# Kernel optimization log

Hardware: AMD Instinct MI355X
Metric: run time of the kernel (lower is better)

## Reference

```python
import jax, jax.numpy as jnp
import numpy as np

N, NFEAT, NHID, NHEADS = 4096, 512, 64, 8
P = 65536
ALPHA = 0.2  # LeakyReLU negative slope
NEG = -9e15  # mask value used by standard dense GAT


def setup_inputs() -> dict:
    key = jax.random.key(0)
    ks = jax.random.split(key, 9)
    x = jax.random.normal(ks[0], (N, NFEAT), dtype=jnp.float32)
    adj = (jax.random.uniform(ks[1], (N, N)) < 0.01).astype(jnp.float32)  # sparse-ish binary graph
    s = 0.05
    W_heads = jax.random.normal(ks[2], (NHEADS, NFEAT, NHID), dtype=jnp.float32) * s
    a_heads = jax.random.normal(ks[3], (NHEADS, 2 * NHID), dtype=jnp.float32) * s
    W_out = jax.random.normal(ks[4], (NHID * NHEADS, NHID), dtype=jnp.float32) * s
    a_out = jax.random.normal(ks[5], (2 * NHID,), dtype=jnp.float32) * s
    W_score = jax.random.normal(ks[6], (NHID, NHID), dtype=jnp.float32) * s
    pair1_idx = jax.random.randint(ks[7], (P,), 0, N, dtype=jnp.int32)
    pair2_idx = jax.random.randint(ks[8], (P,), 0, N, dtype=jnp.int32)
    return dict(x=x, adj=adj, W_heads=W_heads, a_heads=a_heads,
                W_out=W_out, a_out=a_out, W_score=W_score,
                pair1_idx=pair1_idx, pair2_idx=pair2_idx)


def _gat_layer(h, adj, W, a, concat):
    # Standard dense GraphAttentionLayer (no dropout: eval mode)
    Wh = h @ W                       # [N, out]
    out = W.shape[1]
    e_src = Wh @ a[:out]             # [N]
    e_dst = Wh @ a[out:]             # [N]
    e = jax.nn.leaky_relu(e_src[:, None] + e_dst[None, :], ALPHA)  # [N, N]
    logits = jnp.where(adj > 0, e, NEG)
    attn = jax.nn.softmax(logits, axis=1)
    hp = attn @ Wh                   # [N, out]
    return jax.nn.elu(hp) if concat else hp


def reference(x, adj, W_heads, a_heads, W_out, a_out, W_score, pair1_idx, pair2_idx):
    # multi-head layer, vmapped over heads; each head: [N, NHID]
    heads = jax.vmap(lambda W, a: _gat_layer(x, adj, W, a, True))(W_heads, a_heads)
    h = jnp.transpose(heads, (1, 0, 2)).reshape(N, NHEADS * NHID)  # concat dim=1
    h = jax.nn.elu(_gat_layer(h, adj, W_out, a_out, False))        # [N, NHID]
    embed1 = h[pair1_idx]            # sparse.mm(pair1_map, h) == row gather
    embed2 = h[pair2_idx]
    # diag(embed1 @ W_score @ embed2.T) == rowwise dot
    scores = jnp.sum((embed1 @ W_score) * embed2, axis=1)  # [P]
    return scores
```

## Files before the change

kernel.cpp:

```cpp
#include <hip/hip_runtime.h>
#include <math.h>

#define N 4096
#define NFEAT 512
#define NHID 64
#define NHEADS 8
#define P_PAIRS 65536
#define CAP 128
#define LRELU_ALPHA 0.2f
#define GEMM_BLOCKS 256
#define CSR_BLOCKS 512

typedef short bf16x8 __attribute__((ext_vector_type(8)));
typedef float f32x4 __attribute__((ext_vector_type(4)));

__device__ __forceinline__ unsigned short f2bf(float f) {
  unsigned u = __float_as_uint(f);
  u = u + 0x7FFFu + ((u >> 16) & 1u);
  return (unsigned short)(u >> 16);
}
__device__ __forceinline__ float bf2f(unsigned short h) {
  return __uint_as_float(((unsigned)h) << 16);
}

__device__ __forceinline__ int swz(int row, int s) {
  int sl = ((row & 7) * 32 + s) ^ ((row & 7) << 3);
  return (row >> 3) * 256 + sl;
}

__global__ __launch_bounds__(256) void prep_wt(const float* __restrict__ W1,
                                               const float* __restrict__ W2,
                                               unsigned short* __restrict__ w1hi,
                                               unsigned short* __restrict__ w1lo,
                                               unsigned short* __restrict__ w2hi,
                                               unsigned short* __restrict__ w2lo) {
  int c = blockIdx.x;
  const float* W;
  unsigned short *hiP, *loP;
  if (c < 512) { W = W1; hiP = w1hi; loP = w1lo; }
  else         { W = W2; hiP = w2hi; loP = w2lo; c -= 512; }
  const float* Wp = W + (size_t)(c >> 6) * 512 * 64 + (c & 63);
  for (int k = threadIdx.x; k < 512; k += 256) {
    float v = Wp[(size_t)k * 64];
    unsigned short hb = f2bf(v);
    hiP[(size_t)c * 512 + k] = hb;
    loP[(size_t)c * 512 + k] = f2bf(v - bf2f(hb));
  }
}

template <bool F32A>
__device__ __forceinline__ void gemm_body(unsigned short* As, unsigned short* Bs,
                                          int mIdx, int head,
                                          const float* __restrict__ Af,
                                          const unsigned short* __restrict__ Ahi,
                                          const unsigned short* __restrict__ Alo,
                                          const unsigned short* __restrict__ Bhi,
                                          const unsigned short* __restrict__ Blo,
                                          const float* __restrict__ aVec,
                                          float* __restrict__ C,
                                          float* __restrict__ esrc,
                                          float* __restrict__ edst,
                                          float* __restrict__ cpart) {
  const int t = threadIdx.x;
  const int m0 = mIdx * 128;
  const int c0 = head * 64;
  const int lane = t & 63, wave = t >> 6;
  const int g = lane >> 4, r = lane & 15;
  const int wm = (wave >> 1) * 32;
  const int wn = (wave & 1) * 32;
  const int sar = t >> 2, sak = (t & 3) * 8;
  const int tb = t & 255;
  const int sbr = tb >> 2, sbk = (tb & 3) * 8;
  const unsigned short* Bsel = (t < 256) ? Bhi : Blo;
  const int bhalf = (t < 256) ? 0 : 1;
  const int idxA = swz(sar, sak);
  const int idxB = swz(sbr, sbk);
  const size_t aOff = (size_t)(m0 + sar) * 512 + sak;
  const size_t bOff = (size_t)(c0 + sbr) * 512 + sbk;
  const f32x4 z = {0.f, 0.f, 0.f, 0.f};
  f32x4 acc[2][2];
  acc[0][0] = z; acc[0][1] = z; acc[1][0] = z; acc[1][1] = z;

  int4 a0, a1, b0;
  auto loadRegs = [&](int kb) {
    if constexpr (F32A) {
      float4 v0 = *(const float4*)(Af + aOff + kb);
      float4 v1 = *(const float4*)(Af + aOff + kb + 4);
      unsigned h0 = f2bf(v0.x), h1 = f2bf(v0.y), h2 = f2bf(v0.z), h3 = f2bf(v0.w);
      unsigned h4 = f2bf(v1.x), h5 = f2bf(v1.y), h6 = f2bf(v1.z), h7 = f2bf(v1.w);
      unsigned l0 = f2bf(v0.x - bf2f(h0)), l1 = f2bf(v0.y - bf2f(h1));
      unsigned l2 = f2bf(v0.z - bf2f(h2)), l3 = f2bf(v0.w - bf2f(h3));
      unsigned l4 = f2bf(v1.x - bf2f(h4)), l5 = f2bf(v1.y - bf2f(h5));
      unsigned l6 = f2bf(v1.z - bf2f(h6)), l7 = f2bf(v1.w - bf2f(h7));
      a0.x = h0 | (h1 << 16); a0.y = h2 | (h3 << 16);
      a0.z = h4 | (h5 << 16); a0.w = h6 | (h7 << 16);
      a1.x = l0 | (l1 << 16); a1.y = l2 | (l3 << 16);
      a1.z = l4 | (l5 << 16); a1.w = l6 | (l7 << 16);
    } else {
      a0 = *(const int4*)(Ahi + aOff + kb);
      a1 = *(const int4*)(Alo + aOff + kb);
    }
    b0 = *(const int4*)(Bsel + bOff + kb);
  };
  auto storeLds = [&](int buf) {
    *(int4*)(&As[(buf * 2 + 0) * 4096 + idxA]) = a0;
    *(int4*)(&As[(buf * 2 + 1) * 4096 + idxA]) = a1;
    *(int4*)(&Bs[(buf * 2 + bhalf) * 2048 + idxB]) = b0;
  };

  loadRegs(0);
  storeLds(0);
  __syncthreads();

  for (int ch = 0; ch < 16; ++ch) {
    const int cur = ch & 1;
    if (ch < 15) loadRegs((ch + 1) * 32);
    bf16x8 ah[2], al[2], bh[2], bl[2];
#pragma unroll
    for (int f = 0; f < 2; ++f) {
      int ia = swz(wm + f * 16 + r, 8 * g);
      int ib = swz(wn + f * 16 + r, 8 * g);
      ah[f] = *(const bf16x8*)(&As[(cur * 2 + 0) * 4096 + ia]);
      al[f] = *(const bf16x8*)(&As[(cur * 2 + 1) * 4096 + ia]);
      bh[f] = *(const bf16x8*)(&Bs[(cur * 2 + 0) * 2048 + ib]);
      bl[f] = *(const bf16x8*)(&Bs[(cur * 2 + 1) * 2048 + ib]);
    }
#pragma unroll
    for (int i = 0; i < 2; ++i)
#pragma unroll
      for (int j = 0; j < 2; ++j) {
        acc[i][j] = __builtin_amdgcn_mfma_f32_16x16x32_bf16(ah[i], bh[j], acc[i][j], 0, 0, 0);
        acc[i][j] = __builtin_amdgcn_mfma_f32_16x16x32_bf16(al[i], bh[j], acc[i][j], 0, 0, 0);
        acc[i][j] = __builtin_amdgcn_mfma_f32_16x16x32_bf16(ah[i], bl[j], acc[i][j], 0, 0, 0);
      }
    if (ch < 15) {
      storeLds(cur ^ 1);
      __syncthreads();
    }
  }

  __syncthreads();
  float* Cs = (float*)As;
#pragma unroll
  for (int i = 0; i < 2; ++i)
#pragma unroll
    for (int j = 0; j < 2; ++j)
#pragma unroll
      for (int q = 0; q < 4; ++q)
        Cs[(wm + i * 16 + 4 * g + q) * 64 + wn + j * 16 + r] = acc[i][j][q];
  __syncthreads();
  float* Cp = C + ((size_t)head * N + m0) * 64;
  const float* aV = aVec + (size_t)head * 128;
  float as_ = aV[lane], ad_ = aV[64 + lane];
  float cs = 0.f;
#pragma unroll
  for (int rr = 0; rr < 16; ++rr) {
    int row = wave * 16 + rr;
    float v = Cs[row * 64 + lane];
    Cp[(size_t)row * 64 + lane] = v;
    cs += v;
    float s = v * as_, d = v * ad_;
#pragma unroll
    for (int off = 32; off; off >>= 1) {
      s += __shfl_xor(s, off);
      d += __shfl_xor(d, off);
    }
    if (lane == 0) {
      esrc[(size_t)head * N + m0 + row] = s;
      edst[(size_t)head * N + m0 + row] = d;
    }
  }
  float* red = (float*)Bs;
  red[wave * 64 + lane] = cs;
  __syncthreads();
  if (wave == 0) {
    float s = 0.f;
#pragma unroll
    for (int j = 0; j < 8; ++j) s += red[j * 64 + lane];
    cpart[((size_t)head * 32 + mIdx) * 64 + lane] = s;
  }
}

__global__ __launch_bounds__(512) void front(const float* __restrict__ x,
                                             const float* __restrict__ adj,
                                             const unsigned short* __restrict__ w1hi,
                                             const unsigned short* __restrict__ w1lo,
                                             const float* __restrict__ aVec,
                                             float* __restrict__ Wh1,
                                             float* __restrict__ es1,
                                             float* __restrict__ ed1,
                                             float* __restrict__ cpart1,
                                             int* __restrict__ counts,
                                             int* __restrict__ cols) {
  __shared__ unsigned short As[2 * 2 * 4096];
  __shared__ unsigned short Bs[2 * 2 * 2048];
  int b = blockIdx.x;
  if (b >= GEMM_BLOCKS) {
    int lane = threadIdx.x & 63;
    int row = (b - GEMM_BLOCKS) * 8 + (threadIdx.x >> 6);
    const float4* arow = (const float4*)(adj + (size_t)row * N);
    int* crow = cols + (size_t)row * CAP;
    unsigned long long below = (1ULL << lane) - 1;
    int cnt = 0;
#pragma unroll 4
    for (int it = 0; it < 16; ++it) {
      float4 v = arow[it * 64 + lane];
      int base = (it * 64 + lane) * 4;
#pragma unroll
      for (int j = 0; j < 4; ++j) {
        float f = (j == 0) ? v.x : (j == 1) ? v.y : (j == 2) ? v.z : v.w;
        unsigned long long mask = __ballot(f > 0.f);
        if (f > 0.f) {
          int pos = cnt + __popcll(mask & below);
          if (pos < CAP) crow[pos] = base + j;
        }
        cnt += __popcll(mask);
      }
    }
    if (lane == 0) counts[row] = cnt < CAP ? cnt : CAP;
    return;
  }
  gemm_body<true>(As, Bs, b & 31, b >> 5, x, nullptr, nullptr, w1hi, w1lo,
                  aVec, Wh1, es1, ed1, cpart1);
}

__global__ __launch_bounds__(256) void gat_attn_l1(const float* __restrict__ Wh,
                                                   const float* __restrict__ esrc,
                                                   const float* __restrict__ edst,
                                                   const int* __restrict__ counts,
                                                   const int* __restrict__ cols,
                                                   const float* __restrict__ cpart1,
                                                   unsigned short* __restrict__ hhi,
                                                   unsigned short* __restrict__ hlo) {
  int h = blockIdx.x & 7;
  int wv = threadIdx.x >> 6;
  int lane = threadIdx.x & 63;
  int sg = lane >> 4, sl = lane & 15;
  int i = (blockIdx.x >> 3) * 4 + wv;
  int cnt = counts[i];
  __shared__ int jls[4][CAP];
  __shared__ float pls[4][CAP];
  const float* WhH = Wh + (size_t)h * N * 64;
  float4 acc = {0.f, 0.f, 0.f, 0.f};
  if (cnt == 0) {
    float4 sv = {0.f, 0.f, 0.f, 0.f};
    for (int j = 0; j < 32; ++j) {
      float4 p = *(const float4*)(cpart1 + ((size_t)h * 32 + j) * 64 + 4 * sl);
      sv.x += p.x; sv.y += p.y; sv.z += p.z; sv.w += p.w;
    }
    acc.x = sv.x * (1.0f / N); acc.y = sv.y * (1.0f / N);
    acc.z = sv.z * (1.0f / N); acc.w = sv.w * (1.0f / N);
  } else {
    const int* cl = cols + (size_t)i * CAP;
    jls[wv][lane] = (lane < cnt) ? cl[lane] : 0;
    jls[wv][lane + 64] = (lane + 64 < cnt) ? cl[lane + 64] : 0;
    float ei = esrc[h * N + i];
    const float* ed = edst + (size_t)h * N;
    float e0 = -1e30f, e1 = -1e30f;
    if (lane < cnt) {
      float e = ei + ed[jls[wv][lane]];
      e0 = (e > 0.f) ? e : LRELU_ALPHA * e;
    }
    if (lane + 64 < cnt) {
      float e = ei + ed[jls[wv][lane + 64]];
      e1 = (e > 0.f) ? e : LRELU_ALPHA * e;
    }
    float m = fmaxf(e0, e1);
#pragma unroll
    for (int off = 32; off; off >>= 1) m = fmaxf(m, __shfl_xor(m, off));
    float p0 = (lane < cnt) ? __expf(e0 - m) : 0.f;
    float p1 = (lane + 64 < cnt) ? __expf(e1 - m) : 0.f;
    float ssum = p0 + p1;
#pragma unroll
    for (int off = 32; off; off >>= 1) ssum += __shfl_xor(ssum, off);
    pls[wv][lane] = p0;
    pls[wv][lane + 64] = p1;
    int L = (cnt + 15) & ~15;
    for (int k = 0; k < L; k += 16) {
      int j0 = jls[wv][k + sg];
      int j1 = jls[wv][k + 4 + sg];
      int j2 = jls[wv][k + 8 + sg];
      int j3 = jls[wv][k + 12 + sg];
      float4 v0 = *(const float4*)(WhH + ((size_t)j0 << 6) + 4 * sl);
      float4 v1 = *(const float4*)(WhH + ((size_t)j1 << 6) + 4 * sl);
      float4 v2 = *(const float4*)(WhH + ((size_t)j2 << 6) + 4 * sl);
      float4 v3 = *(const float4*)(WhH + ((size_t)j3 << 6) + 4 * sl);
      float q0 = pls[wv][k + sg];
      float q1 = pls[wv][k + 4 + sg];
      float q2 = pls[wv][k + 8 + sg];
      float q3 = pls[wv][k + 12 + sg];
      acc.x = fmaf(q0, v0.x, acc.x); acc.y = fmaf(q0, v0.y, acc.y);
      acc.z = fmaf(q0, v0.z, acc.z); acc.w = fmaf(q0, v0.w, acc.w);
      acc.x = fmaf(q1, v1.x, acc.x); acc.y = fmaf(q1, v1.y, acc.y);
      acc.z = fmaf(q1, v1.z, acc.z); acc.w = fmaf(q1, v1.w, acc.w);
      acc.x = fmaf(q2, v2.x, acc.x); acc.y = fmaf(q2, v2.y, acc.y);
      acc.z = fmaf(q2, v2.z, acc.z); acc.w = fmaf(q2, v2.w, acc.w);
      acc.x = fmaf(q3, v3.x, acc.x); acc.y = fmaf(q3, v3.y, acc.y);
      acc.z = fmaf(q3, v3.z, acc.z); acc.w = fmaf(q3, v3.w, acc.w);
    }
    acc.x += __shfl_xor(acc.x, 16); acc.y += __shfl_xor(acc.y, 16);
    acc.z += __shfl_xor(acc.z, 16); acc.w += __shfl_xor(acc.w, 16);
    acc.x += __shfl_xor(acc.x, 32); acc.y += __shfl_xor(acc.y, 32);
    acc.z += __shfl_xor(acc.z, 32); acc.w += __shfl_xor(acc.w, 32);
    float inv = 1.0f / ssum;
    acc.x *= inv; acc.y *= inv; acc.z *= inv; acc.w *= inv;
  }
  if (sg == 0) {
    acc.x = (acc.x > 0.f) ? acc.x : expm1f(acc.x);
    acc.y = (acc.y > 0.f) ? acc.y : expm1f(acc.y);
    acc.z = (acc.z > 0.f) ? acc.z : expm1f(acc.z);
    acc.w = (acc.w > 0.f) ? acc.w : expm1f(acc.w);
    ushort4 hi4, lo4;
    hi4.x = f2bf(acc.x); lo4.x = f2bf(acc.x - bf2f(hi4.x));
    hi4.y = f2bf(acc.y); lo4.y = f2bf(acc.y - bf2f(hi4.y));
    hi4.z = f2bf(acc.z); lo4.z = f2bf(acc.z - bf2f(hi4.z));
    hi4.w = f2bf(acc.w); lo4.w = f2bf(acc.w - bf2f(hi4.w));
    size_t o = (size_t)i * 512 + h * 64 + 4 * sl;
    *(ushort4*)(hhi + o) = hi4;
    *(ushort4*)(hlo + o) = lo4;
  }
}

__global__ __launch_bounds__(512) void mid(const unsigned short* __restrict__ h1hi,
                                           const unsigned short* __restrict__ h1lo,
                                           const unsigned short* __restrict__ w2hi,
                                           const unsigned short* __restrict__ w2lo,
                                           const float* __restrict__ aVec,
                                           float* __restrict__ Wh2,
                                           float* __restrict__ es2,
                                           float* __restrict__ ed2,
                                           float* __restrict__ cpart2) {
  __shared__ unsigned short As[2 * 2 * 4096];
  __shared__ unsigned short Bs[2 * 2 * 2048];
  gemm_body<false>(As, Bs, blockIdx.x, 0, nullptr, h1hi, h1lo, w2hi, w2lo,
                   aVec, Wh2, es2, ed2, cpart2);
}

__global__ __launch_bounds__(256) void gat_attn_l2(const float* __restrict__ Wh,
                                                   const float* __restrict__ esrc,
                                                   const float* __restrict__ edst,
                                                   const int* __restrict__ counts,
                                                   const int* __restrict__ cols,
                                                   const float* __restrict__ cpart2,
                                                   const float* __restrict__ Wsc,
                                                   float* __restrict__ hf,
                                                   float* __restrict__ g) {
  __shared__ float Ws[64][64];
  int t = threadIdx.x;
#pragma unroll
  for (int j = 0; j < 4; ++j) {
    int q = t + j * 256;
    int k = q >> 4, cq = (q & 15) * 4;
    *(float4*)(&Ws[k][cq]) = *(const float4*)(Wsc + k * 64 + cq);
  }
  __syncthreads();
  int wv = t >> 6;
  int lane = t & 63;
  int sg = lane >> 4, sl = lane & 15;
  int i = (blockIdx.x << 2) + wv;
  int cnt = counts[i];
  __shared__ int jls[4][CAP];
  __shared__ float pls[4][CAP];
  float v;
  if (cnt == 0) {
    float s = 0.f;
    for (int j = 0; j < 32; ++j) s += cpart2[(size_t)j * 64 + lane];
    v = s * (1.0f / N);
  } else {
    const int* cl = cols + (size_t)i * CAP;
    jls[wv][lane] = (lane < cnt) ? cl[lane] : 0;
    jls[wv][lane + 64] = (lane + 64 < cnt) ? cl[lane + 64] : 0;
    float ei = esrc[i];
    float e0 = -1e30f, e1 = -1e30f;
    if (lane < cnt) {
      float e = ei + edst[jls[wv][lane]];
      e0 = (e > 0.f) ? e : LRELU_ALPHA * e;
    }
    if (lane + 64 < cnt) {
      float e = ei + edst[jls[wv][lane + 64]];
      e1 = (e > 0.f) ? e : LRELU_ALPHA * e;
    }
    float m = fmaxf(e0, e1);
#pragma unroll
    for (int off = 32; off; off >>= 1) m = fmaxf(m, __shfl_xor(m, off));
    float p0 = (lane < cnt) ? __expf(e0 - m) : 0.f;
    float p1 = (lane + 64 < cnt) ? __expf(e1 - m) : 0.f;
    float ssum = p0 + p1;
#pragma unroll
    for (int off = 32; off; off >>= 1) ssum += __shfl_xor(ssum, off);
    pls[wv][lane] = p0;
    pls[wv][lane + 64] = p1;
    float4 acc = {0.f, 0.f, 0.f, 0.f};
    int L = (cnt + 15) & ~15;
    for (int k = 0; k < L; k += 16) {
      int j0 = jls[wv][k + sg];
      int j1 = jls[wv][k + 4 + sg];
      int j2 = jls[wv][k + 8 + sg];
      int j3 = jls[wv][k + 12 + sg];
      float4 v0 = *(const float4*)(Wh + ((size_t)j0 << 6) + 4 * sl);
      float4 v1 = *(const float4*)(Wh + ((size_t)j1 << 6) + 4 * sl);
      float4 v2 = *(const float4*)(Wh + ((size_t)j2 << 6) + 4 * sl);
      float4 v3 = *(const float4*)(Wh + ((size_t)j3 << 6) + 4 * sl);
      float q0 = pls[wv][k + sg];
      float q1 = pls[wv][k + 4 + sg];
      float q2 = pls[wv][k + 8 + sg];
      float q3 = pls[wv][k + 12 + sg];
      acc.x = fmaf(q0, v0.x, acc.x); acc.y = fmaf(q0, v0.y, acc.y);
      acc.z = fmaf(q0, v0.z, acc.z); acc.w = fmaf(q0, v0.w, acc.w);
      acc.x = fmaf(q1, v1.x, acc.x); acc.y = fmaf(q1, v1.y, acc.y);
      acc.z = fmaf(q1, v1.z, acc.z); acc.w = fmaf(q1, v1.w, acc.w);
      acc.x = fmaf(q2, v2.x, acc.x); acc.y = fmaf(q2, v2.y, acc.y);
      acc.z = fmaf(q2, v2.z, acc.z); acc.w = fmaf(q2, v2.w, acc.w);
      acc.x = fmaf(q3, v3.x, acc.x); acc.y = fmaf(q3, v3.y, acc.y);
      acc.z = fmaf(q3, v3.z, acc.z); acc.w = fmaf(q3, v3.w, acc.w);
    }
    acc.x += __shfl_xor(acc.x, 16); acc.y += __shfl_xor(acc.y, 16);
    acc.z += __shfl_xor(acc.z, 16); acc.w += __shfl_xor(acc.w, 16);
    acc.x += __shfl_xor(acc.x, 32); acc.y += __shfl_xor(acc.y, 32);
    acc.z += __shfl_xor(acc.z, 32); acc.w += __shfl_xor(acc.w, 32);
    float cx = __shfl(acc.x, lane >> 2);
    float cy = __shfl(acc.y, lane >> 2);
    float cz = __shfl(acc.z, lane >> 2);
    float cw = __shfl(acc.w, lane >> 2);
    int cmp = lane & 3;
    v = (cmp == 0) ? cx : (cmp == 1) ? cy : (cmp == 2) ? cz : cw;
    v /= ssum;
  }
  v = (v > 0.f) ? v : expm1f(v);
  hf[((size_t)i << 6) + lane] = v;
  float gacc = 0.f;
#pragma unroll
  for (int k = 0; k < 64; ++k)
    gacc = fmaf(__shfl(v, k), Ws[k][lane], gacc);
  g[((size_t)i << 6) + lane] = gacc;
}

__global__ __launch_bounds__(256) void score_quad(const float* __restrict__ g,
                                                  const float* __restrict__ hf,
                                                  const int* __restrict__ p1,
                                                  const int* __restrict__ p2,
                                                  float* __restrict__ out) {
  int w = threadIdx.x >> 6;
  int lane = threadIdx.x & 63;
  int sub = lane >> 4, sl = lane & 15;
  int p = (((blockIdx.x << 2) + w) << 2) + sub;
  int i1 = p1[p], i2 = p2[p];
  float4 ga = *(const float4*)(g + ((size_t)i1 << 6) + sl * 4);
  float4 hb = *(const float4*)(hf + ((size_t)i2 << 6) + sl * 4);
  float v = ga.x * hb.x + ga.y * hb.y + ga.z * hb.z + ga.w * hb.w;
#pragma unroll
  for (int off = 8; off; off >>= 1) v += __shfl_xor(v, off);
  if (sl == 0) out[p] = v;
}

extern "C" void kernel_launch(void* const* d_in, const int* in_sizes, int n_in,
                              void* d_out, int out_size, void* d_ws, size_t ws_size,
                              hipStream_t stream) {
  const float* x       = (const float*)d_in[0];
  const float* adj     = (const float*)d_in[1];
  const float* W_heads = (const float*)d_in[2];
  const float* a_heads = (const float*)d_in[3];
  const float* W_out   = (const float*)d_in[4];
  const float* a_out   = (const float*)d_in[5];
  const float* W_score = (const float*)d_in[6];
  const int* p1        = (const int*)d_in[7];
  const int* p2        = (const int*)d_in[8];
  float* out           = (float*)d_out;

  char* ws = (char*)d_ws;
  size_t off = 0;
  auto alloc = [&](size_t bytes) -> void* {
    void* p = ws + off;
    off += (bytes + 255) & ~(size_t)255;
    return p;
  };
  int*   counts = (int*)alloc((size_t)N * 4);
  int*   cols   = (int*)alloc((size_t)N * CAP * 4);
  unsigned short* wt1hi = (unsigned short*)alloc((size_t)512 * 512 * 2);
  unsigned short* wt1lo = (unsigned short*)alloc((size_t)512 * 512 * 2);
  unsigned short* wt2hi = (unsigned short*)alloc((size_t)64 * 512 * 2);
  unsigned short* wt2lo = (unsigned short*)alloc((size_t)64 * 512 * 2);
  float* Wh1    = (float*)alloc((size_t)NHEADS * N * 64 * 4);
  float* es1    = (float*)alloc((size_t)NHEADS * N * 4);
  float* ed1    = (float*)alloc((size_t)NHEADS * N * 4);
  float* cpart1 = (float*)alloc((size_t)NHEADS * 32 * 64 * 4);
  unsigned short* h1hi = (unsigned short*)alloc((size_t)N * 512 * 2);
  unsigned short* h1lo = (unsigned short*)alloc((size_t)N * 512 * 2);
  float* Wh2    = (float*)alloc((size_t)N * 64 * 4);
  float* es2    = (float*)alloc((size_t)N * 4);
  float* ed2    = (float*)alloc((size_t)N * 4);
  float* cpart2 = (float*)alloc((size_t)32 * 64 * 4);
  float* hf     = (float*)alloc((size_t)N * 64 * 4);
  float* g      = (float*)alloc((size_t)N * 64 * 4);

  prep_wt<<<576, 256, 0, stream>>>(W_heads, W_out, wt1hi, wt1lo, wt2hi, wt2lo);

  front<<<GEMM_BLOCKS + CSR_BLOCKS, 512, 0, stream>>>(
      x, adj, wt1hi, wt1lo, a_heads, Wh1, es1, ed1, cpart1, counts, cols);

  gat_attn_l1<<<(N / 4) * NHEADS, 256, 0, stream>>>(Wh1, es1, ed1, counts, cols,
                                                    cpart1, h1hi, h1lo);

  mid<<<32, 512, 0, stream>>>(h1hi, h1lo, wt2hi, wt2lo, a_out, Wh2, es2, ed2,
                              cpart2);

  gat_attn_l2<<<N / 4, 256, 0, stream>>>(Wh2, es2, ed2, counts, cols, cpart2,
                                         W_score, hf, g);

  score_quad<<<P_PAIRS / 16, 256, 0, stream>>>(g, hf, p1, p2, out);
}
```

Before: 86.41 us.

## Fuse layer-2 GEMM, attention and scoring into one persistent kernel with grid barriers

```diff
diff --git a/kernel.cpp b/kernel.cpp
--- a/kernel.cpp
+++ b/kernel.cpp
@@ -10,6 +10,7 @@
 #define LRELU_ALPHA 0.2f
 #define GEMM_BLOCKS 256
 #define CSR_BLOCKS 512
+#define TAIL_BLOCKS 256
 
 typedef short bf16x8 __attribute__((ext_vector_type(8)));
 typedef float f32x4 __attribute__((ext_vector_type(4)));
@@ -33,7 +34,9 @@
                                                unsigned short* __restrict__ w1hi,
                                                unsigned short* __restrict__ w1lo,
                                                unsigned short* __restrict__ w2hi,
-                                               unsigned short* __restrict__ w2lo) {
+                                               unsigned short* __restrict__ w2lo,
+                                               int* __restrict__ barrier) {
+  if (blockIdx.x == 0 && threadIdx.x < 2) barrier[threadIdx.x] = 0;
   int c = blockIdx.x;
   const float* W;
   unsigned short *hiP, *loP;
@@ -321,136 +324,156 @@
   }
 }
 
-__global__ __launch_bounds__(512) void mid(const unsigned short* __restrict__ h1hi,
-                                           const unsigned short* __restrict__ h1lo,
-                                           const unsigned short* __restrict__ w2hi,
-                                           const unsigned short* __restrict__ w2lo,
-                                           const float* __restrict__ aVec,
-                                           float* __restrict__ Wh2,
-                                           float* __restrict__ es2,
-                                           float* __restrict__ ed2,
-                                           float* __restrict__ cpart2) {
-  __shared__ unsigned short As[2 * 2 * 4096];
-  __shared__ unsigned short Bs[2 * 2 * 2048];
-  gemm_body<false>(As, Bs, blockIdx.x, 0, nullptr, h1hi, h1lo, w2hi, w2lo,
-                   aVec, Wh2, es2, ed2, cpart2);
-}
-
-__global__ __launch_bounds__(256) void gat_attn_l2(const float* __restrict__ Wh,
-                                                   const float* __restrict__ esrc,
-                                                   const float* __restrict__ edst,
-                                                   const int* __restrict__ counts,
-                                                   const int* __restrict__ cols,
-                                                   const float* __restrict__ cpart2,
-                                                   const float* __restrict__ Wsc,
-                                                   float* __restrict__ hf,
-                                                   float* __restrict__ g) {
-  __shared__ float Ws[64][64];
-  int t = threadIdx.x;
-#pragma unroll
-  for (int j = 0; j < 4; ++j) {
-    int q = t + j * 256;
-    int k = q >> 4, cq = (q & 15) * 4;
-    *(float4*)(&Ws[k][cq]) = *(const float4*)(Wsc + k * 64 + cq);
-  }
-  __syncthreads();
+__global__ __launch_bounds__(512) void tail2(const unsigned short* __restrict__ h1hi,
+                                             const unsigned short* __restrict__ h1lo,
+                                             const unsigned short* __restrict__ w2hi,
+                                             const unsigned short* __restrict__ w2lo,
+                                             const float* __restrict__ aVec,
+                                             float* __restrict__ Wh2,
+                                             float* __restrict__ es2,
+                                             float* __restrict__ ed2,
+                                             float* __restrict__ cpart2,
+                                             const int* __restrict__ counts,
+                                             const int* __restrict__ cols,
+                                             const float* __restrict__ Wsc,
+                                             const int* __restrict__ p1,
+                                             const int* __restrict__ p2,
+                                             float* __restrict__ hf,
+                                             float* __restrict__ g,
+                                             float* __restrict__ out,
+                                             int* __restrict__ barrier) {
+  __shared__ unsigned char smem[49152];
+  unsigned short* As = (unsigned short*)smem;
+  unsigned short* Bs = (unsigned short*)(smem + 32768);
+  const int t = threadIdx.x;
+
+  if (blockIdx.x < 32)
+    gemm_body<false>(As, Bs, blockIdx.x, 0, nullptr, h1hi, h1lo, w2hi, w2lo,
+                     aVec, Wh2, es2, ed2, cpart2);
+  __syncthreads();
+
+  float* Ws = (float*)smem;
+#pragma unroll
+  for (int j = 0; j < 2; ++j) {
+    int q = t + j * 512;
+    *(float4*)(&Ws[(q >> 4) * 64 + (q & 15) * 4]) =
+        *(const float4*)(Wsc + (q >> 4) * 64 + (q & 15) * 4);
+  }
+
+  __threadfence();
+  if (t == 0) {
+    __hip_atomic_fetch_add(&barrier[0], 1, __ATOMIC_ACQ_REL, __HIP_MEMORY_SCOPE_AGENT);
+    while (__hip_atomic_load(&barrier[0], __ATOMIC_ACQUIRE, __HIP_MEMORY_SCOPE_AGENT) <
+           TAIL_BLOCKS)
+      __builtin_amdgcn_s_sleep(32);
+  }
+  __syncthreads();
+
+  int* jls = (int*)(smem + 16384);
+  float* pls = (float*)(smem + 16384 + 4096);
   int wv = t >> 6;
   int lane = t & 63;
   int sg = lane >> 4, sl = lane & 15;
-  int i = (blockIdx.x << 2) + wv;
-  int cnt = counts[i];
-  __shared__ int jls[4][CAP];
-  __shared__ float pls[4][CAP];
-  float v;
-  if (cnt == 0) {
-    float s = 0.f;
-    for (int j = 0; j < 32; ++j) s += cpart2[(size_t)j * 64 + lane];
-    v = s * (1.0f / N);
-  } else {
-    const int* cl = cols + (size_t)i * CAP;
-    jls[wv][lane] = (lane < cnt) ? cl[lane] : 0;
-    jls[wv][lane + 64] = (lane + 64 < cnt) ? cl[lane + 64] : 0;
-    float ei = esrc[i];
-    float e0 = -1e30f, e1 = -1e30f;
-    if (lane < cnt) {
-      float e = ei + edst[jls[wv][lane]];
-      e0 = (e > 0.f) ? e : LRELU_ALPHA * e;
-    }
-    if (lane + 64 < cnt) {
-      float e = ei + edst[jls[wv][lane + 64]];
-      e1 = (e > 0.f) ? e : LRELU_ALPHA * e;
-    }
-    float m = fmaxf(e0, e1);
-#pragma unroll
-    for (int off = 32; off; off >>= 1) m = fmaxf(m, __shfl_xor(m, off));
-    float p0 = (lane < cnt) ? __expf(e0 - m) : 0.f;
-    float p1 = (lane + 64 < cnt) ? __expf(e1 - m) : 0.f;
-    float ssum = p0 + p1;
-#pragma unroll
-    for (int off = 32; off; off >>= 1) ssum += __shfl_xor(ssum, off);
-    pls[wv][lane] = p0;
-    pls[wv][lane + 64] = p1;
-    float4 acc = {0.f, 0.f, 0.f, 0.f};
-    int L = (cnt + 15) & ~15;
-    for (int k = 0; k < L; k += 16) {
-      int j0 = jls[wv][k + sg];
-      int j1 = jls[wv][k + 4 + sg];
-      int j2 = jls[wv][k + 8 + sg];
-      int j3 = jls[wv][k + 12 + sg];
-      float4 v0 = *(const float4*)(Wh + ((size_t)j0 << 6) + 4 * sl);
-      float4 v1 = *(const float4*)(Wh + ((size_t)j1 << 6) + 4 * sl);
-      float4 v2 = *(const float4*)(Wh + ((size_t)j2 << 6) + 4 * sl);
-      float4 v3 = *(const float4*)(Wh + ((size_t)j3 << 6) + 4 * sl);
-      float q0 = pls[wv][k + sg];
-      float q1 = pls[wv][k + 4 + sg];
-      float q2 = pls[wv][k + 8 + sg];
-      float q3 = pls[wv][k + 12 + sg];
-      acc.x = fmaf(q0, v0.x, acc.x); acc.y = fmaf(q0, v0.y, acc.y);
-      acc.z = fmaf(q0, v0.z, acc.z); acc.w = fmaf(q0, v0.w, acc.w);
-      acc.x = fmaf(q1, v1.x, acc.x); acc.y = fmaf(q1, v1.y, acc.y);
-      acc.z = fmaf(q1, v1.z, acc.z); acc.w = fmaf(q1, v1.w, acc.w);
-      acc.x = fmaf(q2, v2.x, acc.x); acc.y = fmaf(q2, v2.y, acc.y);
-      acc.z = fmaf(q2, v2.z, acc.z); acc.w = fmaf(q2, v2.w, acc.w);
-      acc.x = fmaf(q3, v3.x, acc.x); acc.y = fmaf(q3, v3.y, acc.y);
-      acc.z = fmaf(q3, v3.z, acc.z); acc.w = fmaf(q3, v3.w, acc.w);
-    }
-    acc.x += __shfl_xor(acc.x, 16); acc.y += __shfl_xor(acc.y, 16);
-    acc.z += __shfl_xor(acc.z, 16); acc.w += __shfl_xor(acc.w, 16);
-    acc.x += __shfl_xor(acc.x, 32); acc.y += __shfl_xor(acc.y, 32);
-    acc.z += __shfl_xor(acc.z, 32); acc.w += __shfl_xor(acc.w, 32);
-    float cx = __shfl(acc.x, lane >> 2);
-    float cy = __shfl(acc.y, lane >> 2);
-    float cz = __shfl(acc.z, lane >> 2);
-    float cw = __shfl(acc.w, lane >> 2);
-    int cmp = lane & 3;
-    v = (cmp == 0) ? cx : (cmp == 1) ? cy : (cmp == 2) ? cz : cw;
-    v /= ssum;
-  }
-  v = (v > 0.f) ? v : expm1f(v);
-  hf[((size_t)i << 6) + lane] = v;
-  float gacc = 0.f;
-#pragma unroll
-  for (int k = 0; k < 64; ++k)
-    gacc = fmaf(__shfl(v, k), Ws[k][lane], gacc);
-  g[((size_t)i << 6) + lane] = gacc;
-}
-
-__global__ __launch_bounds__(256) void score_quad(const float* __restrict__ g,
-                                                  const float* __restrict__ hf,
-                                                  const int* __restrict__ p1,
-                                                  const int* __restrict__ p2,
-                                                  float* __restrict__ out) {
-  int w = threadIdx.x >> 6;
-  int lane = threadIdx.x & 63;
-  int sub = lane >> 4, sl = lane & 15;
-  int p = (((blockIdx.x << 2) + w) << 2) + sub;
-  int i1 = p1[p], i2 = p2[p];
-  float4 ga = *(const float4*)(g + ((size_t)i1 << 6) + sl * 4);
-  float4 hb = *(const float4*)(hf + ((size_t)i2 << 6) + sl * 4);
-  float v = ga.x * hb.x + ga.y * hb.y + ga.z * hb.z + ga.w * hb.w;
-#pragma unroll
-  for (int off = 8; off; off >>= 1) v += __shfl_xor(v, off);
-  if (sl == 0) out[p] = v;
+  int* jw = jls + wv * CAP;
+  float* pw = pls + wv * CAP;
+  for (int ii = 0; ii < 2; ++ii) {
+    int i = blockIdx.x * 16 + wv * 2 + ii;
+    int cnt = counts[i];
+    float v;
+    if (cnt == 0) {
+      float s = 0.f;
+      for (int j = 0; j < 32; ++j) s += cpart2[(size_t)j * 64 + lane];
+      v = s * (1.0f / N);
+    } else {
+      const int* cl = cols + (size_t)i * CAP;
+      jw[lane] = (lane < cnt) ? cl[lane] : 0;
+      jw[lane + 64] = (lane + 64 < cnt) ? cl[lane + 64] : 0;
+      float ei = es2[i];
+      float e0 = -1e30f, e1 = -1e30f;
+      if (lane < cnt) {
+        float e = ei + ed2[jw[lane]];
+        e0 = (e > 0.f) ? e : LRELU_ALPHA * e;
+      }
+      if (lane + 64 < cnt) {
+        float e = ei + ed2[jw[lane + 64]];
+        e1 = (e > 0.f) ? e : LRELU_ALPHA * e;
+      }
+      float m = fmaxf(e0, e1);
+#pragma unroll
+      for (int off = 32; off; off >>= 1) m = fmaxf(m, __shfl_xor(m, off));
+      float p0 = (lane < cnt) ? __expf(e0 - m) : 0.f;
+      float p1 = (lane + 64 < cnt) ? __expf(e1 - m) : 0.f;
+      float ssum = p0 + p1;
+#pragma unroll
+      for (int off = 32; off; off >>= 1) ssum += __shfl_xor(ssum, off);
+      pw[lane] = p0;
+      pw[lane + 64] = p1;
+      float4 acc = {0.f, 0.f, 0.f, 0.f};
+      int L = (cnt + 15) & ~15;
+      for (int k = 0; k < L; k += 16) {
+        int j0 = jw[k + sg];
+        int j1 = jw[k + 4 + sg];
+        int j2 = jw[k + 8 + sg];
+        int j3 = jw[k + 12 + sg];
+        float4 v0 = *(const float4*)(Wh2 + ((size_t)j0 << 6) + 4 * sl);
+        float4 v1 = *(const float4*)(Wh2 + ((size_t)j1 << 6) + 4 * sl);
+        float4 v2 = *(const float4*)(Wh2 + ((size_t)j2 << 6) + 4 * sl);
+        float4 v3 = *(const float4*)(Wh2 + ((size_t)j3 << 6) + 4 * sl);
+        float q0 = pw[k + sg];
+        float q1 = pw[k + 4 + sg];
+        float q2 = pw[k + 8 + sg];
+        float q3 = pw[k + 12 + sg];
+        acc.x = fmaf(q0, v0.x, acc.x); acc.y = fmaf(q0, v0.y, acc.y);
+        acc.z = fmaf(q0, v0.z, acc.z); acc.w = fmaf(q0, v0.w, acc.w);
+        acc.x = fmaf(q1, v1.x, acc.x); acc.y = fmaf(q1, v1.y, acc.y);
+        acc.z = fmaf(q1, v1.z, acc.z); acc.w = fmaf(q1, v1.w, acc.w);
+        acc.x = fmaf(q2, v2.x, acc.x); acc.y = fmaf(q2, v2.y, acc.y);
+        acc.z = fmaf(q2, v2.z, acc.z); acc.w = fmaf(q2, v2.w, acc.w);
+        acc.x = fmaf(q3, v3.x, acc.x); acc.y = fmaf(q3, v3.y, acc.y);
+        acc.z = fmaf(q3, v3.z, acc.z); acc.w = fmaf(q3, v3.w, acc.w);
+      }
+      acc.x += __shfl_xor(acc.x, 16); acc.y += __shfl_xor(acc.y, 16);
+      acc.z += __shfl_xor(acc.z, 16); acc.w += __shfl_xor(acc.w, 16);
+      acc.x += __shfl_xor(acc.x, 32); acc.y += __shfl_xor(acc.y, 32);
+      acc.z += __shfl_xor(acc.z, 32); acc.w += __shfl_xor(acc.w, 32);
+      float cx = __shfl(acc.x, lane >> 2);
+      float cy = __shfl(acc.y, lane >> 2);
+      float cz = __shfl(acc.z, lane >> 2);
+      float cw = __shfl(acc.w, lane >> 2);
+      int cmp = lane & 3;
+      v = (cmp == 0) ? cx : (cmp == 1) ? cy : (cmp == 2) ? cz : cw;
+      v /= ssum;
+    }
+    v = (v > 0.f) ? v : expm1f(v);
+    hf[((size_t)i << 6) + lane] = v;
+    float gacc = 0.f;
+#pragma unroll
+    for (int k = 0; k < 64; ++k)
+      gacc = fmaf(__shfl(v, k), Ws[k * 64 + lane], gacc);
+    g[((size_t)i << 6) + lane] = gacc;
+  }
+
+  __syncthreads();
+  __threadfence();
+  if (t == 0) {
+    __hip_atomic_fetch_add(&barrier[1], 1, __ATOMIC_ACQ_REL, __HIP_MEMORY_SCOPE_AGENT);
+    while (__hip_atomic_load(&barrier[1], __ATOMIC_ACQUIRE, __HIP_MEMORY_SCOPE_AGENT) <
+           TAIL_BLOCKS)
+      __builtin_amdgcn_s_sleep(32);
+  }
+  __syncthreads();
+
+#pragma unroll
+  for (int rep = 0; rep < 8; ++rep) {
+    int p = blockIdx.x * 256 + wv * 32 + rep * 4 + sg;
+    int i1 = p1[p], i2 = p2[p];
+    float4 ga = *(const float4*)(g + ((size_t)i1 << 6) + sl * 4);
+    float4 hb = *(const float4*)(hf + ((size_t)i2 << 6) + sl * 4);
+    float s = ga.x * hb.x + ga.y * hb.y + ga.z * hb.z + ga.w * hb.w;
+#pragma unroll
+    for (int off = 8; off; off >>= 1) s += __shfl_xor(s, off);
+    if (sl == 0) out[p] = s;
+  }
 }
 
 extern "C" void kernel_launch(void* const* d_in, const int* in_sizes, int n_in,
@@ -492,8 +515,10 @@
   float* cpart2 = (float*)alloc((size_t)32 * 64 * 4);
   float* hf     = (float*)alloc((size_t)N * 64 * 4);
   float* g      = (float*)alloc((size_t)N * 64 * 4);
-
-  prep_wt<<<576, 256, 0, stream>>>(W_heads, W_out, wt1hi, wt1lo, wt2hi, wt2lo);
+  int*   barrier = (int*)alloc(256);
+
+  prep_wt<<<576, 256, 0, stream>>>(W_heads, W_out, wt1hi, wt1lo, wt2hi, wt2lo,
+                                   barrier);
 
   front<<<GEMM_BLOCKS + CSR_BLOCKS, 512, 0, stream>>>(
       x, adj, wt1hi, wt1lo, a_heads, Wh1, es1, ed1, cpart1, counts, cols);
@@ -501,11 +526,7 @@
   gat_attn_l1<<<(N / 4) * NHEADS, 256, 0, stream>>>(Wh1, es1, ed1, counts, cols,
                                                     cpart1, h1hi, h1lo);
 
-  mid<<<32, 512, 0, stream>>>(h1hi, h1lo, wt2hi, wt2lo, a_out, Wh2, es2, ed2,
-                              cpart2);
-
-  gat_attn_l2<<<N / 4, 256, 0, stream>>>(Wh2, es2, ed2, counts, cols, cpart2,
-                                         W_score, hf, g);
-
-  score_quad<<<P_PAIRS / 16, 256, 0, stream>>>(g, hf, p1, p2, out);
-}
+  tail2<<<TAIL_BLOCKS, 512, 0, stream>>>(h1hi, h1lo, wt2hi, wt2lo, a_out,
+                                         Wh2, es2, ed2, cpart2, counts, cols,
+                                         W_score, p1, p2, hf, g, out, barrier);
+}
```

New measurement: 212.0 us. +145.3%, slower.
